# Kernel optimization log

Measured on AMD Instinct MI355X. Metric: run time of the kernel, lower is better.

## Reference

```python
import jax, jax.numpy as jnp
import numpy as np

TEMP = 0.07
MOMENTUM = 0.2
K = 8192          # number of sampled negatives per row
NUM_CLASSES = 1000
B, N, D = 256, 32768, 2048
NEG_INF = -1e30


def _gumbel(key, shape):
    u = jax.random.uniform(key, shape, minval=1e-6, maxval=1.0)
    return -jnp.log(-jnp.log(u))


def setup_inputs() -> dict:
    key = jax.random.key(0)
    k1, k2, k3, k4, k5 = jax.random.split(key, 5)
    f = jax.random.normal(k1, (B, D), dtype=jnp.float32)
    f_nv = jax.random.normal(k2, (B, D), dtype=jnp.float32)
    # warmed-up memory bank (the real module L2-normalizes rows on update)
    features = jax.random.normal(k3, (N, D), dtype=jnp.float32)
    features = features / jnp.linalg.norm(features, axis=1, keepdims=True)
    labels = jax.random.randint(k4, (N,), 0, NUM_CLASSES)
    indexes = jax.random.randint(k5, (B,), 0, N)
    return {"f": f, "f_nv": f_nv, "features": features,
            "labels": labels, "indexes": indexes}


def reference(f, f_nv, features, labels, indexes):
    rkey = jax.random.key(42)
    kg1, kg2, kg3 = jax.random.split(rkey, 3)
    k = features                                   # [N, D] memory bank snapshot
    bsz = f.shape[0]

    # l_pos = <f_nv_i, k[indexes_i]>
    l_pos = jnp.sum(f_nv * k[indexes], axis=1, keepdims=True)   # [B, 1]

    mat = jnp.matmul(f, k.T)                       # [B, N]
    mat_sim = jnp.matmul(f_nv, k.T)                # [B, N]

    batch_labels = labels[indexes]                 # [B]
    pos_mask = labels[None, :] == batch_labels[:, None]         # [B, N]

    # torch.randperm-based sampling -> vectorized masked Gumbel sampling.
    # argmax of gumbel restricted to mask = uniform draw from masked set;
    # top-K of gumbel restricted to complement = K draws w/o replacement.
    g1 = _gumbel(kg1, (bsz, k.shape[0]))
    g2 = _gumbel(kg2, (bsz, k.shape[0]))
    g3 = _gumbel(kg3, (bsz, k.shape[0]))

    pos_idx_wogan = jnp.argmax(jnp.where(pos_mask, g1, NEG_INF), axis=1)
    positives_wogan = jnp.take_along_axis(mat, pos_idx_wogan[:, None], axis=1)  # [B,1]

    pos_idx = jnp.argmax(jnp.where(pos_mask, g2, NEG_INF), axis=1)
    positives = jnp.take_along_axis(mat_sim, pos_idx[:, None], axis=1)          # [B,1]

    _, neg_idx = jax.lax.top_k(jnp.where(pos_mask, NEG_INF, g3), K)             # [B,K]
    negatives = jnp.take_along_axis(mat_sim, neg_idx, axis=1)                   # [B,K]

    def ce_target0(logits):
        # CrossEntropyLoss with all targets == 0
        return -jax.nn.log_softmax(logits, axis=1)[:, 0].mean()

    self_out = jnp.concatenate([l_pos, negatives], axis=1) / TEMP
    inter_out = jnp.concatenate([positives, negatives], axis=1) / TEMP
    inter_out_wogan = jnp.concatenate([positives_wogan, negatives], axis=1) / TEMP

    memory_loss = ce_target0(self_out) + ce_target0(inter_out) + ce_target0(inter_out_wogan)

    # no-grad momentum update of the bank (F.normalize uses eps=1e-12)
    upd = MOMENTUM * k[indexes] + (1.0 - MOMENTUM) * f
    upd = upd / jnp.maximum(jnp.linalg.norm(upd, axis=1, keepdims=True), 1e-12)
    new_features = jax.lax.stop_gradient(features.at[indexes].set(upd))

    return memory_loss, new_features
```

## Files before the change

kernel.cpp:

```cpp
#include <hip/hip_runtime.h>
#include <stdint.h>

#define TEMP      0.07f
#define BATCH     256
#define NROWS     32768
#define DIM       2048
#define KNEG      8192

typedef __attribute__((ext_vector_type(8))) short bf16x8;
typedef __attribute__((ext_vector_type(4))) float f32x4;

__host__ __device__ inline void tf2x32(uint32_t ka, uint32_t kb,
                                       uint32_t x0, uint32_t x1,
                                       uint32_t& o0, uint32_t& o1) {
  uint32_t ks2 = ka ^ kb ^ 0x1BD11BDAu;
#define TFR(r) { x0 += x1; x1 = (x1 << r) | (x1 >> (32 - r)); x1 ^= x0; }
  x0 += ka; x1 += kb;
  TFR(13) TFR(15) TFR(26) TFR(6)
  x0 += kb;  x1 += ks2 + 1u;
  TFR(17) TFR(29) TFR(16) TFR(24)
  x0 += ks2; x1 += ka + 2u;
  TFR(13) TFR(15) TFR(26) TFR(6)
  x0 += ka;  x1 += kb + 3u;
  TFR(17) TFR(29) TFR(16) TFR(24)
  x0 += kb;  x1 += ks2 + 4u;
  TFR(13) TFR(15) TFR(26) TFR(6)
  x0 += ks2; x1 += ka + 5u;
#undef TFR
  o0 = x0; o1 = x1;
}

__device__ inline uint32_t ubits_at(uint32_t ka, uint32_t kb, uint32_t q) {
  uint32_t a, b; tf2x32(ka, kb, 0u, q, a, b);
  return (a ^ b) >> 9;
}

__device__ inline float block_sum(float v, float* sm) {
  __syncthreads();
  const int lane = threadIdx.x & 63;
  const int w = threadIdx.x >> 6;
  const int nw = blockDim.x >> 6;
  for (int o = 32; o; o >>= 1) v += __shfl_down(v, o, 64);
  if (lane == 0) sm[w] = v;
  __syncthreads();
  if (w == 0) {
    float x = (lane < nw) ? sm[lane] : 0.f;
    for (int o = 8; o; o >>= 1) x += __shfl_down(x, o, 64);
    if (lane == 0) sm[0] = x;
  }
  __syncthreads();
  return sm[0];
}

__device__ inline uint32_t pk2(float a, float b) {
  uint32_t ua = __float_as_uint(a), ub = __float_as_uint(b);
  ua = (ua + 0x7FFFu + ((ua >> 16) & 1u)) >> 16;
  ub = (ub + 0x7FFFu + ((ub >> 16) & 1u)) >> 16;
  return ua | (ub << 16);
}

__global__ __launch_bounds__(256) void cvtA(const float* __restrict__ A,
                                            uint32_t* __restrict__ Abf) {
  const int t = threadIdx.x;
  const int w = blockIdx.x * 4 + (t >> 6);
  const int l = t & 63;
  const int mt = w >> 6, kt = w & 63;
  const float* src = &A[(size_t)(mt * 16 + (l & 15)) * DIM + kt * 32 + (l >> 4) * 8];
  float4 f0 = *(const float4*)src;
  float4 f1 = *(const float4*)(src + 4);
  *(uint4*)(Abf + (size_t)w * 256 + l * 4) =
      make_uint4(pk2(f0.x, f0.y), pk2(f0.z, f0.w), pk2(f1.x, f1.y), pk2(f1.z, f1.w));
}

#define BN2 32
#define BK2 64
#define NT2 (DIM / BK2)

__global__ __launch_bounds__(256, 4) void gemm_fused(
    const uint32_t* __restrict__ Abf,
    const float* __restrict__ B,
    float* __restrict__ C,
    float* __restrict__ outF,
    int skip) {
  __shared__ uint32_t Bs[2][BN2 * BK2 / 2];
  const int t = threadIdx.x;
  const int bn = blockIdx.x;
  const int l = t & 63, w = t >> 6;
  const int sr = t >> 3, sg = t & 7;
  const size_t srcRow = (size_t)(bn * BN2 + sr) * DIM;
  const int swslot = (sr * 32) + ((sg ^ (sr & 7)) * 4);

  float4 b0, b1;
  f32x4 acc[4][2] = {};

#define SLOAD(k0) {                                                            \
    b0 = *(const float4*)&B[srcRow + (k0) + sg * 8];                           \
    b1 = *(const float4*)&B[srcRow + (k0) + sg * 8 + 4]; }

#define SWRITE(buf) {                                                          \
    *(uint4*)&Bs[buf][swslot] = make_uint4(pk2(b0.x, b0.y), pk2(b0.z, b0.w),   \
                                           pk2(b1.x, b1.y), pk2(b1.z, b1.w)); }

#define SOUT(k0) {                                                             \
    int g = bn * BN2 + sr;                                                     \
    if (g >= skip) {                                                           \
      float* d = &outF[(size_t)g * DIM + (k0) + sg * 8];                       \
      d[0] = b0.x; d[1] = b0.y; d[2] = b0.z; d[3] = b0.w;                      \
      d[4] = b1.x; d[5] = b1.y; d[6] = b1.z; d[7] = b1.w; } }

#define COMPUTE(buf, t0) {                                                     \
    _Pragma("unroll")                                                          \
    for (int kk = 0; kk < 2; ++kk) {                                           \
      bf16x8 af[4];                                                            \
      _Pragma("unroll")                                                        \
      for (int m = 0; m < 4; ++m) {                                            \
        int mt = w * 4 + m;                                                    \
        af[m] = *(const bf16x8*)(Abf +                                         \
                 ((size_t)(mt * 64 + ((t0) * 2 + kk)) * 64 + l) * 4);          \
      }                                                                        \
      bf16x8 bfr[2];                                                           \
      _Pragma("unroll")                                                        \
      for (int n = 0; n < 2; ++n) {                                            \
        int r = n * 16 + (l & 15);                                             \
        int slot = (kk * 4 + (l >> 4)) ^ (r & 7);                              \
        bfr[n] = *(const bf16x8*)&Bs[buf][r * 32 + slot * 4];                  \
      }                                                                        \
      _Pragma("unroll")                                                        \
      for (int m = 0; m < 4; ++m)                                              \
        _Pragma("unroll")                                                      \
        for (int n = 0; n < 2; ++n)                                            \
          acc[m][n] = __builtin_amdgcn_mfma_f32_16x16x32_bf16(                 \
              af[m], bfr[n], acc[m][n], 0, 0, 0);                              \
    } }

  SLOAD(0); SWRITE(0); SOUT(0);
  __syncthreads();
  for (int t0 = 0; t0 < NT2; ++t0) {
    const int cur = t0 & 1;
    if (t0 + 1 < NT2) SLOAD((t0 + 1) * BK2);
    __builtin_amdgcn_sched_barrier(0);
    COMPUTE(cur, t0);
    if (t0 + 1 < NT2) { SWRITE(1 - cur); SOUT((t0 + 1) * BK2); }
    __syncthreads();
  }

  const int colb = bn * BN2 + (l & 15);
#pragma unroll
  for (int m = 0; m < 4; ++m)
#pragma unroll
    for (int n = 0; n < 2; ++n) {
      size_t base = (size_t)(w * 64 + m * 16 + (l >> 4) * 4) * NROWS + colb + n * 16;
#pragma unroll
      for (int r = 0; r < 4; ++r)
        C[base + (size_t)r * NROWS] = acc[m][n][r];
    }
#undef SLOAD
#undef SWRITE
#undef SOUT
#undef COMPUTE
}

__global__ __launch_bounds__(1024) void sample_loss(
    const float* __restrict__ f, const float* __restrict__ f_nv,
    const float* __restrict__ features, const int* __restrict__ labels,
    const int* __restrict__ indexes, const float* __restrict__ mat_sim,
    float* __restrict__ row_loss,
    uint32_t k1a, uint32_t k1b, uint32_t k2a, uint32_t k2b,
    uint32_t k3a, uint32_t k3b) {
  __shared__ uint32_t keys[NROWS];
  __shared__ uint32_t hist4[4][256];
  __shared__ uint32_t hist[256];
  __shared__ unsigned long long am1, am2;
  __shared__ int tie_j[128];
  __shared__ int tie_cnt;
  __shared__ float sred[16];
  __shared__ float swm[16], sws[16];
  __shared__ uint32_t bc_prefix, bc_rem;
  __shared__ int blab_s;

  const int t = threadIdx.x;
  const int i = blockIdx.x;
  const size_t mbase = (size_t)i * NROWS;

  if (t == 0) {
    blab_s = labels[indexes[i]];
    am1 = 0ull; am2 = 0ull; tie_cnt = 0;
  }
  __syncthreads();
  const int blab = blab_s;

#pragma unroll 2
  for (int s = 0; s < NROWS / 1024; ++s) {
    int j = t + 1024 * s;
    uint32_t q = (uint32_t)i * NROWS + (uint32_t)j;
    int lab = labels[j];
    if (lab == blab) {
      keys[j] = 0u;
      unsigned long long lo = (unsigned long long)(uint32_t)(NROWS - 1 - j);
      uint32_t u1 = ubits_at(k1a, k1b, q);
      uint32_t u2 = ubits_at(k2a, k2b, q);
      atomicMax(&am1, ((unsigned long long)u1 << 32) | lo);
      atomicMax(&am2, ((unsigned long long)u2 << 32) | lo);
    } else {
      keys[j] = ubits_at(k3a, k3b, q);
    }
  }
  __syncthreads();

  const int jw = NROWS - 1 - (int)(unsigned)(am1 & 0xFFFFFFFFull);
  const int jp = NROWS - 1 - (int)(unsigned)(am2 & 0xFFFFFFFFull);

  const int bank = indexes[i];
  float d1 = 0.f, d2 = 0.f, d3 = 0.f;
  for (int d = t; d < DIM; d += 1024) {
    float fnv = f_nv[(size_t)i * DIM + d];
    d1 += fnv * features[(size_t)bank * DIM + d];
    d2 += f[(size_t)i * DIM + d] * features[(size_t)jw * DIM + d];
    d3 += fnv * features[(size_t)jp * DIM + d];
  }
  const float l_pos = block_sum(d1, sred);
  const float posw  = block_sum(d2, sred);
  const float posv  = block_sum(d3, sred);

  uint32_t prefix = 0, remaining = KNEG;
  const int shifts[3] = {15, 7, 0};
  const int nbits[3]  = {8, 8, 7};
  for (int p = 0; p < 3; ++p) {
    const int sh = shifts[p];
    const int nb = 1 << nbits[p];
    ((uint32_t*)hist4)[t] = 0u;
    __syncthreads();
    const int hsel = t >> 8;
    for (int s = 0; s < NROWS / 1024; ++s) {
      int j = t + 1024 * s;
      uint32_t k = keys[j];
      bool ok = (p == 0) || ((k >> (sh + nbits[p])) == prefix);
      if (ok) atomicAdd(&hist4[hsel][(k >> sh) & (uint32_t)(nb - 1)], 1u);
    }
    __syncthreads();
    if (t < nb) hist[t] = hist4[0][t] + hist4[1][t] + hist4[2][t] + hist4[3][t];
    __syncthreads();
    if (t == 0) {
      uint32_t c = 0; int b = nb - 1;
      for (;; --b) {
        c += hist[b];
        if (c >= remaining || b == 0) break;
      }
      bc_prefix = (prefix << nbits[p]) | (uint32_t)b;
      bc_rem = remaining - (c - hist[b]);
    }
    __syncthreads();
    prefix = bc_prefix; remaining = bc_rem;
  }
  const uint32_t T = prefix;
  const uint32_t need = remaining;

  float m = -INFINITY, ssum = 0.f;
  for (int s = 0; s < NROWS / 1024; ++s) {
    int j = t + 1024 * s;
    uint32_t k = keys[j];
    if (k > T) {
      float v = mat_sim[mbase + j] / TEMP;
      if (v <= m) ssum += expf(v - m);
      else { ssum = ssum * expf(m - v) + 1.0f; m = v; }
    } else if (k == T) {
      int p = atomicAdd(&tie_cnt, 1);
      if (p < 128) tie_j[p] = j;
    }
  }
  for (int o = 32; o; o >>= 1) {
    float m2 = __shfl_down(m, o, 64);
    float s2 = __shfl_down(ssum, o, 64);
    if (m2 > m) { ssum = ssum * expf(m - m2) + s2; m = m2; }
    else if (m2 != -INFINITY) ssum += s2 * expf(m2 - m);
  }
  if ((t & 63) == 0) { swm[t >> 6] = m; sws[t >> 6] = ssum; }
  __syncthreads();
  if (t < 64) {
    float mm = (t < 16) ? swm[t] : -INFINITY;
    float ss = (t < 16) ? sws[t] : 0.f;
    for (int o = 8; o; o >>= 1) {
      float m2 = __shfl_down(mm, o, 64);
      float s2 = __shfl_down(ss, o, 64);
      if (m2 > mm) { ss = ss * expf(mm - m2) + s2; mm = m2; }
      else if (m2 != -INFINITY) ss += s2 * expf(m2 - mm);
    }
    if (t == 0) { swm[0] = mm; sws[0] = ss; }
  }
  __syncthreads();

  if (t == 0) {
    float M = swm[0], S = sws[0];
    int tc = tie_cnt;
    if (tc <= 128) {
      for (int a2 = 1; a2 < tc; ++a2) {
        int v = tie_j[a2]; int b2 = a2 - 1;
        while (b2 >= 0 && tie_j[b2] > v) { tie_j[b2 + 1] = tie_j[b2]; --b2; }
        tie_j[b2 + 1] = v;
      }
      for (uint32_t r = 0; r < need; ++r) {
        float v = mat_sim[mbase + tie_j[r]] / TEMP;
        if (v <= M) S += expf(v - M);
        else { S = S * expf(M - v) + 1.0f; M = v; }
      }
    } else {
      uint32_t taken = 0;
      for (int j = 0; j < NROWS && taken < need; ++j) {
        if (keys[j] == T) {
          float v = mat_sim[mbase + j] / TEMP;
          if (v <= M) S += expf(v - M);
          else { S = S * expf(M - v) + 1.0f; M = v; }
          ++taken;
        }
      }
    }
    float lp = l_pos / TEMP, pv = posv / TEMP, pw = posw / TEMP;
    float L = 0.f;
    { float X = fmaxf(M, lp); L += X + logf(expf(lp - X) + S * expf(M - X)) - lp; }
    { float X = fmaxf(M, pv); L += X + logf(expf(pv - X) + S * expf(M - X)) - pv; }
    { float X = fmaxf(M, pw); L += X + logf(expf(pw - X) + S * expf(M - X)) - pw; }
    row_loss[i] = L;
  }
}

__global__ void finalize_loss(const float* __restrict__ row_loss,
                              float* __restrict__ out) {
  __shared__ float sm[4];
  int t = threadIdx.x;
  float v = row_loss[t];
  for (int o = 32; o; o >>= 1) v += __shfl_down(v, o, 64);
  if ((t & 63) == 0) sm[t >> 6] = v;
  __syncthreads();
  if (t == 0) out[0] = (sm[0] + sm[1] + sm[2] + sm[3]) * (1.0f / BATCH);
}

__global__ void copy_front(const float* __restrict__ src,
                           float* __restrict__ dst, int n4) {
  int idx = blockIdx.x * blockDim.x + threadIdx.x;
  int stride = gridDim.x * blockDim.x;
  for (int i = idx; i < n4; i += stride) {
    float4 v = *(const float4*)&src[(size_t)i * 4];
    float* d = &dst[(size_t)i * 4];
    d[0] = v.x; d[1] = v.y; d[2] = v.z; d[3] = v.w;
  }
}

__global__ __launch_bounds__(256) void update_rows(
    const float* __restrict__ f, const float* __restrict__ features,
    const int* __restrict__ indexes, float* __restrict__ outF) {
  __shared__ float sred[16];
  const int i = blockIdx.x;
  const int row = indexes[i];
  for (int i2 = i + 1; i2 < BATCH; ++i2)
    if (indexes[i2] == row) return;
  const int t = threadIdx.x;
  float ss = 0.f;
  for (int d = t; d < DIM; d += 256) {
    float u = 0.2f * features[(size_t)row * DIM + d] + 0.8f * f[(size_t)i * DIM + d];
    ss += u * u;
  }
  ss = block_sum(ss, sred);
  float nrm = fmaxf(sqrtf(ss), 1e-12f);
  for (int d = t; d < DIM; d += 256) {
    float u = 0.2f * features[(size_t)row * DIM + d] + 0.8f * f[(size_t)i * DIM + d];
    outF[(size_t)row * DIM + d] = u / nrm;
  }
}

extern "C" void kernel_launch(void* const* d_in, const int* in_sizes, int n_in,
                              void* d_out, int out_size, void* d_ws, size_t ws_size,
                              hipStream_t stream) {
  (void)in_sizes; (void)n_in; (void)out_size;
  const float* f        = (const float*)d_in[0];
  const float* f_nv     = (const float*)d_in[1];
  const float* features = (const float*)d_in[2];
  const int*   labels   = (const int*)d_in[3];
  const int*   indexes  = (const int*)d_in[4];
  float* out = (float*)d_out;

  const size_t need = ((size_t)BATCH * NROWS + 256 + 262144) * sizeof(float);
  float* mat_sim;
  float* row_loss;
  uint32_t* Abf;
  int skip_rows;
  bool use_ws = (d_ws != nullptr) && (ws_size >= need);
  if (use_ws) {
    mat_sim = (float*)d_ws;
    row_loss = mat_sim + (size_t)BATCH * NROWS;
    Abf = (uint32_t*)(row_loss + 256);
    skip_rows = 0;
  } else {
    mat_sim = out + 4;
    row_loss = mat_sim + (size_t)BATCH * NROWS;
    Abf = (uint32_t*)(row_loss + 256);
    skip_rows = 4352;
  }

  uint32_t c[6];
  { uint32_t a, b;
    tf2x32(0u, 42u, 0u, 0u, a, b); c[0] = a; c[1] = b;
    tf2x32(0u, 42u, 0u, 1u, a, b); c[2] = a; c[3] = b;
    tf2x32(0u, 42u, 0u, 2u, a, b); c[4] = a; c[5] = b; }

  cvtA<<<dim3(256), dim3(256), 0, stream>>>(f_nv, Abf);
  gemm_fused<<<dim3(NROWS / BN2), dim3(256), 0, stream>>>(
      Abf, features, mat_sim, out + 1, skip_rows);
  sample_loss<<<dim3(BATCH), dim3(1024), 0, stream>>>(
      f, f_nv, features, labels, indexes, mat_sim, row_loss,
      c[0], c[1], c[2], c[3], c[4], c[5]);
  finalize_loss<<<dim3(1), dim3(256), 0, stream>>>(row_loss, out);
  if (!use_ws) {
    copy_front<<<dim3(2048), dim3(256), 0, stream>>>(
        features, out + 1, 4352 * DIM / 4);
  }
  update_rows<<<dim3(BATCH), dim3(256), 0, stream>>>(f, features, indexes, out + 1);
}
```

Measured before the change: 299.4 us.

## Pipeline GEMM B tiles via direct global-to-LDS loads and fuse first histogram pass

After: 348.1 us. 16.3% more time.

```diff
diff --git a/kernel.cpp b/kernel.cpp
--- a/kernel.cpp
+++ b/kernel.cpp
@@ -72,76 +72,110 @@
       make_uint4(pk2(f0.x, f0.y), pk2(f0.z, f0.w), pk2(f1.x, f1.y), pk2(f1.z, f1.w));
 }
 
+__device__ inline void gll16(const float* g, float* l) {
+  __builtin_amdgcn_global_load_lds(
+      (const __attribute__((address_space(1))) uint32_t*)g,
+      (__attribute__((address_space(3))) uint32_t*)l, 16, 0, 0);
+}
+
+__device__ inline bf16x8 bfragf32(const float* bp, int r, int g0) {
+  const int x = r & 7;
+  const float4 u = *(const float4*)(bp + r * 64 + ((g0 ^ x) << 2));
+  const float4 v = *(const float4*)(bp + r * 64 + (((g0 + 1) ^ x) << 2));
+  uint32_t w0, w1, w2, w3;
+  asm("v_cvt_pk_bf16_f32 %0, %1, %2" : "=v"(w0) : "v"(u.x), "v"(u.y));
+  asm("v_cvt_pk_bf16_f32 %0, %1, %2" : "=v"(w1) : "v"(u.z), "v"(u.w));
+  asm("v_cvt_pk_bf16_f32 %0, %1, %2" : "=v"(w2) : "v"(v.x), "v"(v.y));
+  asm("v_cvt_pk_bf16_f32 %0, %1, %2" : "=v"(w3) : "v"(v.z), "v"(v.w));
+  union { uint32_t u4[4]; bf16x8 b; } cv;
+  cv.u4[0] = w0; cv.u4[1] = w1; cv.u4[2] = w2; cv.u4[3] = w3;
+  return cv.b;
+}
+
 #define BN2 32
 #define BK2 64
 #define NT2 (DIM / BK2)
 
 __global__ __launch_bounds__(256, 4) void gemm_fused(
     const uint32_t* __restrict__ Abf,
-    const float* __restrict__ B,
+    const float* __restrict__ Bfeat,
     float* __restrict__ C,
     float* __restrict__ outF,
     int skip) {
-  __shared__ uint32_t Bs[2][BN2 * BK2 / 2];
+  __shared__ float Bs[3][BN2 * BK2];
+  __shared__ float pad[256];
   const int t = threadIdx.x;
   const int bn = blockIdx.x;
   const int l = t & 63, w = t >> 6;
-  const int sr = t >> 3, sg = t & 7;
-  const size_t srcRow = (size_t)(bn * BN2 + sr) * DIM;
-  const int swslot = (sr * 32) + ((sg ^ (sr & 7)) * 4);
-
-  float4 b0, b1;
+
   f32x4 acc[4][2] = {};
-
-#define SLOAD(k0) {                                                            \
-    b0 = *(const float4*)&B[srcRow + (k0) + sg * 8];                           \
-    b1 = *(const float4*)&B[srcRow + (k0) + sg * 8 + 4]; }
-
-#define SWRITE(buf) {                                                          \
-    *(uint4*)&Bs[buf][swslot] = make_uint4(pk2(b0.x, b0.y), pk2(b0.z, b0.w),   \
-                                           pk2(b1.x, b1.y), pk2(b1.z, b1.w)); }
-
-#define SOUT(k0) {                                                             \
-    int g = bn * BN2 + sr;                                                     \
-    if (g >= skip) {                                                           \
-      float* d = &outF[(size_t)g * DIM + (k0) + sg * 8];                       \
-      d[0] = b0.x; d[1] = b0.y; d[2] = b0.z; d[3] = b0.w;                      \
-      d[4] = b1.x; d[5] = b1.y; d[6] = b1.z; d[7] = b1.w; } }
-
-#define COMPUTE(buf, t0) {                                                     \
+  bf16x8 afA[4], afB[4];
+
+#define AFRAG(mt, kidx) \
+  (*(const bf16x8*)(Abf + ((size_t)((mt) * 64 + (kidx)) * 256 + l * 4)))
+
+#define STAGE(K) {                                                             \
+    const int kb_ = (K) * BK2;                                                 \
+    float* db_ = &Bs[(K) % 3][0];                                              \
     _Pragma("unroll")                                                          \
-    for (int kk = 0; kk < 2; ++kk) {                                           \
-      bf16x8 af[4];                                                            \
+    for (int i_ = 0; i_ < 2; ++i_) {                                           \
+      const int r_ = w * 8 + i_ * 4 + (l >> 4);                                \
+      const float* gp_ = &Bfeat[(size_t)(bn * BN2 + r_) * DIM + kb_ +          \
+                                (((l & 15) ^ (r_ & 7)) << 2)];                 \
+      gll16(gp_, db_ + (w * 2 + i_) * 256);                                    \
+    } }
+
+#pragma unroll
+  for (int m = 0; m < 4; ++m) afA[m] = AFRAG(w * 4 + m, 0);
+  __builtin_amdgcn_sched_barrier(0);
+  STAGE(0);
+  __builtin_amdgcn_sched_barrier(0);
+  STAGE(1);
+  { const float* jp = (const float*)((const char*)Bfeat + l * 16);
+    gll16(jp, pad); gll16(jp, pad); }
+
+#define BODY(T, AC, AN) {                                                      \
+    asm volatile("s_waitcnt vmcnt(4)" ::: "memory");                           \
+    __builtin_amdgcn_s_barrier();                                              \
+    const int tt_ = (T);                                                       \
+    const float* bc_ = &Bs[tt_ % 3][0];                                        \
+    bf16x8 a1_[4];                                                             \
+    _Pragma("unroll")                                                          \
+    for (int m = 0; m < 4; ++m) a1_[m] = AFRAG(w * 4 + m, tt_ * 2 + 1);        \
+    { const int tn_ = (tt_ + 1 < NT2) ? tt_ + 1 : tt_;                         \
+      _Pragma("unroll")                                                        \
+      for (int m = 0; m < 4; ++m) (AN)[m] = AFRAG(w * 4 + m, tn_ * 2); }       \
+    __builtin_amdgcn_sched_barrier(0);                                         \
+    if (tt_ + 2 < NT2) STAGE(tt_ + 2);                                         \
+    _Pragma("unroll")                                                          \
+    for (int i_ = 0; i_ < 2; ++i_) {                                           \
+      const int r_ = w * 8 + i_ * 4 + (l >> 4);                                \
+      const int g_ = bn * BN2 + r_;                                            \
+      f32x4 cv_ = *(const f32x4*)(bc_ + (w * 2 + i_) * 256 + l * 4);           \
+      if (g_ >= skip) {                                                        \
+        float* dp_ = &outF[(size_t)g_ * DIM + tt_ * BK2 +                      \
+                           (((l & 15) ^ (r_ & 7)) << 2)];                      \
+        __builtin_nontemporal_store(cv_, (f32x4*)dp_);                         \
+      } }                                                                      \
+    { bf16x8 b0_ = bfragf32(bc_, (l & 15), (l >> 4) * 2);                      \
+      bf16x8 b1_ = bfragf32(bc_, 16 + (l & 15), (l >> 4) * 2);                 \
       _Pragma("unroll")                                                        \
       for (int m = 0; m < 4; ++m) {                                            \
-        int mt = w * 4 + m;                                                    \
-        af[m] = *(const bf16x8*)(Abf +                                         \
-                 ((size_t)(mt * 64 + ((t0) * 2 + kk)) * 64 + l) * 4);          \
-      }                                                                        \
-      bf16x8 bfr[2];                                                           \
+        acc[m][0] = __builtin_amdgcn_mfma_f32_16x16x32_bf16((AC)[m], b0_, acc[m][0], 0, 0, 0); \
+        acc[m][1] = __builtin_amdgcn_mfma_f32_16x16x32_bf16((AC)[m], b1_, acc[m][1], 0, 0, 0); \
+      } }                                                                      \
+    { bf16x8 b0_ = bfragf32(bc_, (l & 15), 8 + (l >> 4) * 2);                  \
+      bf16x8 b1_ = bfragf32(bc_, 16 + (l & 15), 8 + (l >> 4) * 2);             \
       _Pragma("unroll")                                                        \
-      for (int n = 0; n < 2; ++n) {                                            \
-        int r = n * 16 + (l & 15);                                             \
-        int slot = (kk * 4 + (l >> 4)) ^ (r & 7);                              \
-        bfr[n] = *(const bf16x8*)&Bs[buf][r * 32 + slot * 4];                  \
-      }                                                                        \
-      _Pragma("unroll")                                                        \
-      for (int m = 0; m < 4; ++m)                                              \
-        _Pragma("unroll")                                                      \
-        for (int n = 0; n < 2; ++n)                                            \
-          acc[m][n] = __builtin_amdgcn_mfma_f32_16x16x32_bf16(                 \
-              af[m], bfr[n], acc[m][n], 0, 0, 0);                              \
-    } }
-
-  SLOAD(0); SWRITE(0); SOUT(0);
-  __syncthreads();
-  for (int t0 = 0; t0 < NT2; ++t0) {
-    const int cur = t0 & 1;
-    if (t0 + 1 < NT2) SLOAD((t0 + 1) * BK2);
-    __builtin_amdgcn_sched_barrier(0);
-    COMPUTE(cur, t0);
-    if (t0 + 1 < NT2) { SWRITE(1 - cur); SOUT((t0 + 1) * BK2); }
-    __syncthreads();
+      for (int m = 0; m < 4; ++m) {                                            \
+        acc[m][0] = __builtin_amdgcn_mfma_f32_16x16x32_bf16(a1_[m], b0_, acc[m][0], 0, 0, 0); \
+        acc[m][1] = __builtin_amdgcn_mfma_f32_16x16x32_bf16(a1_[m], b1_, acc[m][1], 0, 0, 0); \
+      } }                                                                      \
+  }
+
+  for (int t0 = 0; t0 < NT2; t0 += 2) {
+    BODY(t0, afA, afB);
+    BODY(t0 + 1, afB, afA);
   }
 
   const int colb = bn * BN2 + (l & 15);
@@ -152,12 +186,11 @@
       size_t base = (size_t)(w * 64 + m * 16 + (l >> 4) * 4) * NROWS + colb + n * 16;
 #pragma unroll
       for (int r = 0; r < 4; ++r)
-        C[base + (size_t)r * NROWS] = acc[m][n][r];
-    }
-#undef SLOAD
-#undef SWRITE
-#undef SOUT
-#undef COMPUTE
+        __builtin_nontemporal_store(acc[m][n][r], &C[base + (size_t)r * NROWS]);
+    }
+#undef STAGE
+#undef AFRAG
+#undef BODY
 }
 
 __global__ __launch_bounds__(1024) void sample_loss(
@@ -186,24 +219,29 @@
     blab_s = labels[indexes[i]];
     am1 = 0ull; am2 = 0ull; tie_cnt = 0;
   }
+  ((uint32_t*)hist4)[t] = 0u;
   __syncthreads();
   const int blab = blab_s;
+  const int hsel = t >> 8;
 
 #pragma unroll 2
   for (int s = 0; s < NROWS / 1024; ++s) {
     int j = t + 1024 * s;
     uint32_t q = (uint32_t)i * NROWS + (uint32_t)j;
     int lab = labels[j];
+    uint32_t key;
     if (lab == blab) {
-      keys[j] = 0u;
+      key = 0u;
       unsigned long long lo = (unsigned long long)(uint32_t)(NROWS - 1 - j);
       uint32_t u1 = ubits_at(k1a, k1b, q);
       uint32_t u2 = ubits_at(k2a, k2b, q);
       atomicMax(&am1, ((unsigned long long)u1 << 32) | lo);
       atomicMax(&am2, ((unsigned long long)u2 << 32) | lo);
     } else {
-      keys[j] = ubits_at(k3a, k3b, q);
-    }
+      key = ubits_at(k3a, k3b, q);
+    }
+    keys[j] = key;
+    atomicAdd(&hist4[hsel][key >> 15], 1u);
   }
   __syncthreads();
 
@@ -228,14 +266,15 @@
   for (int p = 0; p < 3; ++p) {
     const int sh = shifts[p];
     const int nb = 1 << nbits[p];
-    ((uint32_t*)hist4)[t] = 0u;
-    __syncthreads();
-    const int hsel = t >> 8;
-    for (int s = 0; s < NROWS / 1024; ++s) {
-      int j = t + 1024 * s;
-      uint32_t k = keys[j];
-      bool ok = (p == 0) || ((k >> (sh + nbits[p])) == prefix);
-      if (ok) atomicAdd(&hist4[hsel][(k >> sh) & (uint32_t)(nb - 1)], 1u);
+    if (p) {
+      ((uint32_t*)hist4)[t] = 0u;
+      __syncthreads();
+      for (int s = 0; s < NROWS / 1024; ++s) {
+        int j = t + 1024 * s;
+        uint32_t k = keys[j];
+        if ((k >> (sh + nbits[p])) == prefix)
+          atomicAdd(&hist4[hsel][(k >> sh) & (uint32_t)(nb - 1)], 1u);
+      }
     }
     __syncthreads();
     if (t < nb) hist[t] = hist4[0][t] + hist4[1][t] + hist4[2][t] + hist4[3][t];
@@ -339,7 +378,7 @@
   int idx = blockIdx.x * blockDim.x + threadIdx.x;
   int stride = gridDim.x * blockDim.x;
   for (int i = idx; i < n4; i += stride) {
-    float4 v = *(const float4*)&src[(size_t)i * 4];
+    f32x4 v = *(const f32x4*)&src[(size_t)i * 4];
     float* d = &dst[(size_t)i * 4];
     d[0] = v.x; d[1] = v.y; d[2] = v.z; d[3] = v.w;
   }
```

## Load B fragments directly into registers in GEMM and fuse first radix histogram

Applied to the files above, without the earlier changes.

Result: slower. 435.8 us (+45.6%).

```diff
diff --git a/kernel.cpp b/kernel.cpp
--- a/kernel.cpp
+++ b/kernel.cpp
@@ -72,92 +72,71 @@
       make_uint4(pk2(f0.x, f0.y), pk2(f0.z, f0.w), pk2(f1.x, f1.y), pk2(f1.z, f1.w));
 }
 
-#define BN2 32
-#define BK2 64
-#define NT2 (DIM / BK2)
-
-__global__ __launch_bounds__(256, 4) void gemm_fused(
+__global__ __launch_bounds__(256, 4) void gemm_direct(
     const uint32_t* __restrict__ Abf,
-    const float* __restrict__ B,
+    const float* __restrict__ Bfeat,
     float* __restrict__ C,
     float* __restrict__ outF,
     int skip) {
-  __shared__ uint32_t Bs[2][BN2 * BK2 / 2];
   const int t = threadIdx.x;
-  const int bn = blockIdx.x;
   const int l = t & 63, w = t >> 6;
-  const int sr = t >> 3, sg = t & 7;
-  const size_t srcRow = (size_t)(bn * BN2 + sr) * DIM;
-  const int swslot = (sr * 32) + ((sg ^ (sr & 7)) * 4);
-
-  float4 b0, b1;
-  f32x4 acc[4][2] = {};
-
-#define SLOAD(k0) {                                                            \
-    b0 = *(const float4*)&B[srcRow + (k0) + sg * 8];                           \
-    b1 = *(const float4*)&B[srcRow + (k0) + sg * 8 + 4]; }
-
-#define SWRITE(buf) {                                                          \
-    *(uint4*)&Bs[buf][swslot] = make_uint4(pk2(b0.x, b0.y), pk2(b0.z, b0.w),   \
-                                           pk2(b1.x, b1.y), pk2(b1.z, b1.w)); }
-
-#define SOUT(k0) {                                                             \
-    int g = bn * BN2 + sr;                                                     \
-    if (g >= skip) {                                                           \
-      float* d = &outF[(size_t)g * DIM + (k0) + sg * 8];                       \
-      d[0] = b0.x; d[1] = b0.y; d[2] = b0.z; d[3] = b0.w;                      \
-      d[4] = b1.x; d[5] = b1.y; d[6] = b1.z; d[7] = b1.w; } }
-
-#define COMPUTE(buf, t0) {                                                     \
-    _Pragma("unroll")                                                          \
-    for (int kk = 0; kk < 2; ++kk) {                                           \
-      bf16x8 af[4];                                                            \
-      _Pragma("unroll")                                                        \
-      for (int m = 0; m < 4; ++m) {                                            \
-        int mt = w * 4 + m;                                                    \
-        af[m] = *(const bf16x8*)(Abf +                                         \
-                 ((size_t)(mt * 64 + ((t0) * 2 + kk)) * 64 + l) * 4);          \
-      }                                                                        \
-      bf16x8 bfr[2];                                                           \
-      _Pragma("unroll")                                                        \
-      for (int n = 0; n < 2; ++n) {                                            \
-        int r = n * 16 + (l & 15);                                             \
-        int slot = (kk * 4 + (l >> 4)) ^ (r & 7);                              \
-        bfr[n] = *(const bf16x8*)&Bs[buf][r * 32 + slot * 4];                  \
-      }                                                                        \
-      _Pragma("unroll")                                                        \
-      for (int m = 0; m < 4; ++m)                                              \
-        _Pragma("unroll")                                                      \
-        for (int n = 0; n < 2; ++n)                                            \
-          acc[m][n] = __builtin_amdgcn_mfma_f32_16x16x32_bf16(                 \
-              af[m], bfr[n], acc[m][n], 0, 0, 0);                              \
-    } }
-
-  SLOAD(0); SWRITE(0); SOUT(0);
-  __syncthreads();
-  for (int t0 = 0; t0 < NT2; ++t0) {
-    const int cur = t0 & 1;
-    if (t0 + 1 < NT2) SLOAD((t0 + 1) * BK2);
-    __builtin_amdgcn_sched_barrier(0);
-    COMPUTE(cur, t0);
-    if (t0 + 1 < NT2) { SWRITE(1 - cur); SOUT((t0 + 1) * BK2); }
-    __syncthreads();
-  }
-
-  const int colb = bn * BN2 + (l & 15);
+  const int mh = w & 1;
+  const int n0 = blockIdx.x * 32 + (w >> 1) * 16;
+  const int row = n0 + (l & 15);
+  const int kg = (l >> 4) * 8;
+  const float* bsrc = &Bfeat[(size_t)row * DIM + kg];
+  float* bdst = &outF[(size_t)row * DIM + kg];
+  const bool do_copy = (mh == 0) && (row >= skip);
+  const int mh8 = mh * 8;
+
+  f32x4 acc[8] = {};
+  f32x4 b0a, b0b, b1a, b1b, b2a, b2b, b3a, b3b;
+
+#define BLOAD(LA, LB, KS) {                                                  \
+    LA = *(const f32x4*)(bsrc + (KS) * 32);                                  \
+    LB = *(const f32x4*)(bsrc + (KS) * 32 + 4); }
+
+#define AFRAGP(MT, KS) \
+  (*(const bf16x8*)(Abf + (size_t)((MT) * 64 + (KS)) * 256 + l * 4))
+
+#define STEP(CA, CB, LA, LB, KS) {                                           \
+    if ((KS) + 2 < DIM / 32) { BLOAD(LA, LB, (KS) + 2); }                    \
+    uint32_t cw0, cw1, cw2, cw3;                                             \
+    asm("v_cvt_pk_bf16_f32 %0, %1, %2" : "=v"(cw0) : "v"(CA[0]), "v"(CA[1]));\
+    asm("v_cvt_pk_bf16_f32 %0, %1, %2" : "=v"(cw1) : "v"(CA[2]), "v"(CA[3]));\
+    asm("v_cvt_pk_bf16_f32 %0, %1, %2" : "=v"(cw2) : "v"(CB[0]), "v"(CB[1]));\
+    asm("v_cvt_pk_bf16_f32 %0, %1, %2" : "=v"(cw3) : "v"(CB[2]), "v"(CB[3]));\
+    union { uint32_t u[4]; bf16x8 v; } bf_;                                  \
+    bf_.u[0] = cw0; bf_.u[1] = cw1; bf_.u[2] = cw2; bf_.u[3] = cw3;          \
+    if (do_copy) {                                                           \
+      __builtin_nontemporal_store(CA, (f32x4*)(bdst + (KS) * 32));           \
+      __builtin_nontemporal_store(CB, (f32x4*)(bdst + (KS) * 32 + 4));       \
+    }                                                                        \
+    _Pragma("unroll")                                                        \
+    for (int m_ = 0; m_ < 8; ++m_)                                           \
+      acc[m_] = __builtin_amdgcn_mfma_f32_16x16x32_bf16(                     \
+          AFRAGP(mh8 + m_, KS), bf_.v, acc[m_], 0, 0, 0);                    \
+  }
+
+  BLOAD(b0a, b0b, 0);
+  BLOAD(b1a, b1b, 1);
+  for (int ks = 0; ks < DIM / 32; ks += 4) {
+    STEP(b0a, b0b, b2a, b2b, ks);
+    STEP(b1a, b1b, b3a, b3b, ks + 1);
+    STEP(b2a, b2b, b0a, b0b, ks + 2);
+    STEP(b3a, b3b, b1a, b1b, ks + 3);
+  }
+
 #pragma unroll
-  for (int m = 0; m < 4; ++m)
+  for (int m = 0; m < 8; ++m) {
+    size_t base = (size_t)(mh * 128 + m * 16 + (l >> 4) * 4) * NROWS + n0 + (l & 15);
 #pragma unroll
-    for (int n = 0; n < 2; ++n) {
-      size_t base = (size_t)(w * 64 + m * 16 + (l >> 4) * 4) * NROWS + colb + n * 16;
-#pragma unroll
-      for (int r = 0; r < 4; ++r)
-        C[base + (size_t)r * NROWS] = acc[m][n][r];
-    }
-#undef SLOAD
-#undef SWRITE
-#undef SOUT
-#undef COMPUTE
+    for (int r = 0; r < 4; ++r)
+      C[base + (size_t)r * NROWS] = acc[m][r];
+  }
+#undef BLOAD
+#undef AFRAGP
+#undef STEP
 }
 
 __global__ __launch_bounds__(1024) void sample_loss(
@@ -186,24 +165,29 @@
     blab_s = labels[indexes[i]];
     am1 = 0ull; am2 = 0ull; tie_cnt = 0;
   }
+  ((uint32_t*)hist4)[t] = 0u;
   __syncthreads();
   const int blab = blab_s;
+  const int hsel = t >> 8;
 
 #pragma unroll 2
   for (int s = 0; s < NROWS / 1024; ++s) {
     int j = t + 1024 * s;
     uint32_t q = (uint32_t)i * NROWS + (uint32_t)j;
     int lab = labels[j];
+    uint32_t key;
     if (lab == blab) {
-      keys[j] = 0u;
+      key = 0u;
       unsigned long long lo = (unsigned long long)(uint32_t)(NROWS - 1 - j);
       uint32_t u1 = ubits_at(k1a, k1b, q);
       uint32_t u2 = ubits_at(k2a, k2b, q);
       atomicMax(&am1, ((unsigned long long)u1 << 32) | lo);
       atomicMax(&am2, ((unsigned long long)u2 << 32) | lo);
     } else {
-      keys[j] = ubits_at(k3a, k3b, q);
-    }
+      key = ubits_at(k3a, k3b, q);
+    }
+    keys[j] = key;
+    atomicAdd(&hist4[hsel][key >> 15], 1u);
   }
   __syncthreads();
 
@@ -228,14 +212,15 @@
   for (int p = 0; p < 3; ++p) {
     const int sh = shifts[p];
     const int nb = 1 << nbits[p];
-    ((uint32_t*)hist4)[t] = 0u;
-    __syncthreads();
-    const int hsel = t >> 8;
-    for (int s = 0; s < NROWS / 1024; ++s) {
-      int j = t + 1024 * s;
-      uint32_t k = keys[j];
-      bool ok = (p == 0) || ((k >> (sh + nbits[p])) == prefix);
-      if (ok) atomicAdd(&hist4[hsel][(k >> sh) & (uint32_t)(nb - 1)], 1u);
+    if (p) {
+      ((uint32_t*)hist4)[t] = 0u;
+      __syncthreads();
+      for (int s = 0; s < NROWS / 1024; ++s) {
+        int j = t + 1024 * s;
+        uint32_t k = keys[j];
+        if ((k >> (sh + nbits[p])) == prefix)
+          atomicAdd(&hist4[hsel][(k >> sh) & (uint32_t)(nb - 1)], 1u);
+      }
     }
     __syncthreads();
     if (t < nb) hist[t] = hist4[0][t] + hist4[1][t] + hist4[2][t] + hist4[3][t];
@@ -339,9 +324,9 @@
   int idx = blockIdx.x * blockDim.x + threadIdx.x;
   int stride = gridDim.x * blockDim.x;
   for (int i = idx; i < n4; i += stride) {
-    float4 v = *(const float4*)&src[(size_t)i * 4];
+    f32x4 v = *(const f32x4*)&src[(size_t)i * 4];
     float* d = &dst[(size_t)i * 4];
-    d[0] = v.x; d[1] = v.y; d[2] = v.z; d[3] = v.w;
+    d[0] = v[0]; d[1] = v[1]; d[2] = v[2]; d[3] = v[3];
   }
 }
 
@@ -403,7 +388,7 @@
     tf2x32(0u, 42u, 0u, 2u, a, b); c[4] = a; c[5] = b; }
 
   cvtA<<<dim3(256), dim3(256), 0, stream>>>(f_nv, Abf);
-  gemm_fused<<<dim3(NROWS / BN2), dim3(256), 0, stream>>>(
+  gemm_direct<<<dim3(NROWS / 32), dim3(256), 0, stream>>>(
       Abf, features, mat_sim, out + 1, skip_rows);
   sample_loss<<<dim3(BATCH), dim3(1024), 0, stream>>>(
       f, f_nv, features, labels, indexes, mat_sim, row_loss,
```
